# Kernel tuning notes

Hardware: AMD Instinct MI355X
Metric: run time of the kernel (lower is better)

The kernel has to match this reference:

```python
import jax, jax.numpy as jnp
import numpy as np
from jax.scipy.special import gammaln

NSTEP, NGRID, MU, LENF = 730, 1500, 16, 15
PRECS = 1e-5

# [low, high] physical ranges for the 12 HBV parameters (same order as torch code)
PARA_SCALE = np.array([[1, 6], [50, 1000], [0.05, 0.9], [0.01, 0.5], [0.001, 0.2],
                       [0.2, 1], [0, 10], [0, 100], [-2.5, 2.5], [0.5, 10],
                       [0, 0.1], [0, 0.2]], dtype=np.float32)
ROUT_SCALE = np.array([[0, 2.9], [0, 6.5]], dtype=np.float32)


def setup_inputs() -> dict:
    key = jax.random.key(0)
    kp, kt, ke, kpar, krt = jax.random.split(key, 5)
    P = jax.random.uniform(kp, (NSTEP, NGRID), jnp.float32) * 10.0   # precip mm/day
    T = jax.random.normal(kt, (NSTEP, NGRID), jnp.float32) * 8.0     # temp degC
    ETp = jax.random.uniform(ke, (NSTEP, NGRID), jnp.float32) * 5.0  # PET mm/day
    x = jnp.stack([P, T, ETp], axis=-1)                              # [Nstep, Ngrid, 3]
    parameters = jax.random.uniform(kpar, (NGRID, 12, MU), jnp.float32)
    rtwts = jax.random.uniform(krt, (NGRID, 2), jnp.float32)
    return {"x": x, "parameters": parameters, "rtwts": rtwts, "mu": MU}


def _hbv(x, parameters, rtwts, mu):
    Nstep, Ngrid = x.shape[0], x.shape[1]
    # scale raw [0,1] parameters into physical ranges; each is [Ngrid, mu]
    lo, hi = PARA_SCALE[:, 0], PARA_SCALE[:, 1]
    par = [lo[i] + parameters[:, i, :] * (hi[i] - lo[i]) for i in range(12)]
    (parBETA, parFC, parK0, parK1, parK2, parLP, parPERC, parUZL,
     parTT, parCFMAX, parCFR, parCWH) = par

    P, T, ETp = x[:, :, 0], x[:, :, 1], x[:, :, 2]  # each [Nstep, Ngrid]

    init = tuple(jnp.full((Ngrid, mu), 0.001, jnp.float32) for _ in range(5))

    def step(carry, inp):
        SNOWPACK, MELTWATER, SM, SUZ, SLZ = carry
        Pt, Tt, Et = inp
        Pm, Tm, ETpm = Pt[:, None], Tt[:, None], Et[:, None]  # [Ngrid, 1]
        is_rain = (Tm >= parTT).astype(jnp.float32)
        RAIN = Pm * is_rain
        SNOW = Pm * (1.0 - is_rain)
        SNOWPACK = SNOWPACK + SNOW
        melt = jnp.minimum(jnp.maximum(parCFMAX * (Tm - parTT), 0.0), SNOWPACK)
        MELTWATER = MELTWATER + melt
        SNOWPACK = SNOWPACK - melt
        refreezing = jnp.minimum(jnp.maximum(parCFR * parCFMAX * (parTT - Tm), 0.0), MELTWATER)
        SNOWPACK = SNOWPACK + refreezing
        MELTWATER = MELTWATER - refreezing
        tosoil = jnp.maximum(MELTWATER - parCWH * SNOWPACK, 0.0)
        MELTWATER = MELTWATER - tosoil
        soil_wetness = jnp.clip((SM / parFC) ** parBETA, 0.0, 1.0)
        recharge = (RAIN + tosoil) * soil_wetness
        SM = SM + RAIN + tosoil - recharge
        excess = jnp.maximum(SM - parFC, 0.0)
        SM = SM - excess
        evapfactor = jnp.clip(SM / (parLP * parFC), 0.0, 1.0)
        ETact = jnp.minimum(SM, ETpm * evapfactor)
        SM = jnp.maximum(SM - ETact, PRECS)
        SUZ = SUZ + recharge + excess
        PERC = jnp.minimum(SUZ, parPERC)
        SUZ = SUZ - PERC
        Q0 = parK0 * jnp.maximum(SUZ - parUZL, 0.0)
        SUZ = SUZ - Q0
        Q1 = parK1 * SUZ
        SUZ = SUZ - Q1
        SLZ = SLZ + PERC
        Q2 = parK2 * SLZ
        SLZ = SLZ - Q2
        return (SNOWPACK, MELTWATER, SM, SUZ, SLZ), (Q0 + Q1 + Q2, Q0, Q1, Q2, ETact)

    _, (Qsimmu, Q0s, Q1s, Q2s, ETmu) = jax.lax.scan(step, init, (P, T, ETp))

    Qsimave = Qsimmu.mean(-1)  # [Nstep, Ngrid]  (muwts is None)

    # gamma unit hydrograph routing (routOpt=True, comprout=False)
    tempa = ROUT_SCALE[0, 0] + rtwts[:, 0] * (ROUT_SCALE[0, 1] - ROUT_SCALE[0, 0])
    tempb = ROUT_SCALE[1, 0] + rtwts[:, 1] * (ROUT_SCALE[1, 1] - ROUT_SCALE[1, 0])
    aa = jnp.maximum(tempa, 0.0) + 0.1      # [Ngrid]
    theta = jnp.maximum(tempb, 0.0) + 0.5   # [Ngrid]
    t = jnp.arange(LENF, dtype=jnp.float32) + 0.5  # [lenF]
    # w[k, g] = t_k^(a-1) * exp(-t_k/theta) / (Gamma(a) * theta^a)
    w = (jnp.exp(-gammaln(aa))[None, :] * theta[None, :] ** (-aa[None, :])
         * t[:, None] ** (aa[None, :] - 1.0) * jnp.exp(-t[:, None] / theta[None, :]))
    w = w / w.sum(0)  # normalize over kernel axis -> [lenF, Ngrid]

    # causal depthwise conv over time: Qs[n,g] = sum_k w[k,g] * Qsimave[n-k,g]
    xpad = jnp.pad(Qsimave, ((LENF - 1, 0), (0, 0)))
    Qs = jnp.zeros_like(Qsimave)
    for k in range(LENF):
        Qs = Qs + w[k][None, :] * jax.lax.dynamic_slice_in_dim(xpad, LENF - 1 - k, Nstep, 0)
    Qs = Qs[..., None]  # [Nstep, Ngrid, 1]

    Qall = jnp.concatenate([Qs,
                            Q0s.mean(-1, keepdims=True),
                            Q1s.mean(-1, keepdims=True),
                            Q2s.mean(-1, keepdims=True),
                            ETmu.mean(-1, keepdims=True)], axis=-1)
    return Qall  # [Nstep, Ngrid, 5]


def reference(x, parameters, rtwts, mu):
    return _hbv(x, parameters, rtwts, mu)
```

## Files before the change

### kernel.cpp

```cpp
#include <hip/hip_runtime.h>
#include <math.h>

#define NSTEP  730
#define NGRID  1500
#define LENF   15
#define PRECS  1e-5f
#define CH     16
#define NCHUNK 46
#define NPHASE (NCHUNK+3)
#define QROW   260
#define OTW    21

static __device__ __forceinline__ float fast_pow01(float x, float y) {
    return __builtin_amdgcn_exp2f(y * __builtin_amdgcn_logf(x));
}

__global__ __launch_bounds__(256, 1)
void hbv_scan_kernel(const float* __restrict__ x,
                     const float* __restrict__ params,
                     const float* __restrict__ rtwts,
                     float* __restrict__ out)
{
    __shared__ float  xring[3*CH*16];
    __shared__ float  rtbuf[2*CH*64];
    __shared__ float2 soilbuf[2*CH*64];
    __shared__ float  qbuf[2*CH*QROW];
    __shared__ float  outtile[CH*OTW];
    __shared__ float  ring[4*64];

    const int tid  = threadIdx.x;
    const int wid  = tid >> 6;
    const int lane = tid & 63;
    const int gl = lane >> 4, m = lane & 15;
    const int b  = blockIdx.x;
    const int g  = b*4 + gl;
    const float inv16 = 1.f/16.f;

    if (wid == 3) {
        #pragma unroll
        for (int j = 0; j < 3; ++j) {
            const int idx = lane + 64*j;
            const int r = idx/12, rem = idx - 12*r;
            const int gi = rem/3, ch = rem - 3*gi;
            xring[r*16 + gi*4 + ch] = x[r*4500 + b*12 + gi*3 + ch];
        }
    }
    ring[tid & 255] = 0.f;
    __syncthreads();

    if (wid == 0) {
        const float pTT     = -2.5f + params[(g*12+8)*16+m]*5.f;
        const float pCFMAX  =  0.5f + params[(g*12+9)*16+m]*9.5f;
        const float pCFR    =          params[(g*12+10)*16+m]*0.1f;
        const float pCWH    =          params[(g*12+11)*16+m]*0.2f;
        const float refCoef = pCFR*pCFMAX;
        const float negCMTT = -pCFMAX*pTT;
        const float refCTT  = refCoef*pTT;
        float SP = 0.001f, MW = 0.001f;
        for (int p = 0; p < NPHASE; ++p) {
            if (p < NCHUNK) {
                const float* xb = &xring[(p%3)*CH*16 + gl*4];
                float* rb = &rtbuf[(p&1)*CH*64];
                #pragma unroll
                for (int s = 0; s < CH; ++s) {
                    const float2 PT = *(const float2*)(xb + s*16);
                    const float Pm = PT.x, Tm = PT.y;
                    const float RAIN    = (Tm >= pTT) ? Pm : 0.f;
                    const float SNOW    = Pm - RAIN;
                    const float meltcap = fmaxf(fmaf(pCFMAX, Tm, negCMTT), 0.f);
                    const float refcap  = fmaxf(fmaf(-refCoef, Tm, refCTT), 0.f);
                    const float SP1 = SP + SNOW;
                    const float melt = fminf(meltcap, SP1);
                    const float MW1 = MW + melt;
                    const float refreeze = fminf(refcap, MW1);
                    SP = SP1 - melt + refreeze;
                    const float MW2 = MW1 - refreeze;
                    const float tosoil = fmaxf(fmaf(-pCWH, SP, MW2), 0.f);
                    MW = MW2 - tosoil;
                    rb[s*64 + lane] = RAIN + tosoil;
                }
            }
            __syncthreads();
        }
    } else if (wid == 1) {
        const float pBETA = 1.f  + params[(g*12+0)*16+m]*5.f;
        const float pFC   = 50.f + params[(g*12+1)*16+m]*950.f;
        const float pLP   = 0.2f + params[(g*12+5)*16+m]*0.8f;
        const float invFC = 1.f/pFC, invLPFC = 1.f/(pLP*pFC);
        float SM = 0.001f;
        for (int p = 0; p < NPHASE; ++p) {
            if (p >= 1 && p-1 < NCHUNK) {
                const int c = p-1;
                const float* xe = &xring[(c%3)*CH*16 + gl*4 + 2];
                const float* rb = &rtbuf[(c&1)*CH*64];
                float2* sb = &soilbuf[(c&1)*CH*64];
                #pragma unroll
                for (int s = 0; s < CH; ++s) {
                    const float rt = rb[s*64 + lane];
                    const float Em = xe[s*16];
                    const float sw = fminf(fast_pow01(SM*invFC, pBETA), 1.f);
                    const float recharge = rt*sw;
                    const float SM1 = fmaf(rt, 1.f - sw, SM);
                    const float SM2 = fminf(SM1, pFC);
                    const float excess = SM1 - SM2;
                    const float evap = fminf(SM2*invLPFC, 1.f);
                    const float ETact = fminf(SM2, Em*evap);
                    SM = fmaxf(SM2 - ETact, PRECS);
                    sb[s*64 + lane] = make_float2(recharge + excess, ETact);
                }
            }
            __syncthreads();
        }
    } else if (wid == 2) {
        const float pK0   = 0.05f  + params[(g*12+2)*16+m]*0.85f;
        const float pK1   = 0.01f  + params[(g*12+3)*16+m]*0.49f;
        const float pK2   = 0.001f + params[(g*12+4)*16+m]*0.199f;
        const float pPERC =          params[(g*12+6)*16+m]*10.f;
        const float pUZL  =          params[(g*12+7)*16+m]*100.f;
        const float oneMinusK0 = 1.f - pK0, K0UZL = pK0*pUZL;
        float SUZ = 0.001f, SLZ = 0.001f;
        for (int p = 0; p < NPHASE; ++p) {
            if (p >= 2 && p-2 < NCHUNK) {
                const int c = p-2;
                const float2* sb = &soilbuf[(c&1)*CH*64];
                float* qb = &qbuf[(c&1)*CH*QROW];
                #pragma unroll
                for (int s = 0; s < CH; ++s) {
                    const float2 rE = sb[s*64 + lane];
                    const float SUZ1 = SUZ + rE.x;
                    const float SUZ2 = fmaxf(SUZ1 - pPERC, 0.f);
                    const float PERC = SUZ1 - SUZ2;
                    const float SUZ3 = fminf(SUZ2, fmaf(SUZ2, oneMinusK0, K0UZL));
                    const float Q0 = SUZ2 - SUZ3;
                    const float Q1 = pK1 * SUZ3;
                    SUZ = SUZ3 - Q1;
                    const float SLZ1 = SLZ + PERC;
                    const float Q2 = pK2 * SLZ1;
                    SLZ = SLZ1 - Q2;
                    *(float4*)&qb[s*QROW + lane*4] = make_float4(Q0, Q1, Q2, rE.y);
                }
            }
            __syncthreads();
        }
    } else {
        float wq[LENF];
        {
            const float ta  = rtwts[g*2+0] * 2.9f;
            const float tbv = rtwts[g*2+1] * 6.5f;
            const float aa = fmaxf(ta, 0.f) + 0.1f;
            const float th = fmaxf(tbv, 0.f) + 0.5f;
            const float c0v = expf(-lgammaf(aa)) * powf(th, -aa);
            float wsum = 0.f;
            #pragma unroll
            for (int k = 0; k < LENF; ++k) {
                const float tt = (float)k + 0.5f;
                wq[k] = c0v * powf(tt, aa-1.f) * expf(-tt/th);
                wsum += wq[k];
            }
            const float ws = inv16 / wsum;
            #pragma unroll
            for (int k = 0; k < LENF; ++k) wq[k] *= ws;
        }
        int rbase[3], bcol[3], lslot[3];
        #pragma unroll
        for (int j = 0; j < 3; ++j) {
            const int idx = lane + 64*j;
            const int r = idx/12, rem = idx - 12*r;
            const int gi = rem/3, ch = rem - 3*gi;
            rbase[j] = r;
            bcol[j]  = b*12 + gi*3 + ch;
            lslot[j] = r*16 + gi*4 + ch;
        }
        int st_o[5], st_g[5];
        #pragma unroll
        for (int j = 0; j < 5; ++j) {
            const int idx = lane + 64*j;
            const int tt = idx/20, cl = idx - 20*tt;
            st_o[j] = tt*OTW + cl;
            st_g[j] = tt*7500 + cl;
        }

        for (int p = 0; p < NPHASE; ++p) {
            const bool do_stage = (p+1 < NCHUNK);
            float stg0=0.f, stg1=0.f, stg2=0.f;
            if (do_stage) {
                int r0 = (p+1)*CH + rbase[0]; r0 = (r0 < NSTEP) ? r0 : (NSTEP-1);
                int r1 = (p+1)*CH + rbase[1]; r1 = (r1 < NSTEP) ? r1 : (NSTEP-1);
                int r2 = (p+1)*CH + rbase[2]; r2 = (r2 < NSTEP) ? r2 : (NSTEP-1);
                stg0 = x[r0*4500 + bcol[0]];
                stg1 = x[r1*4500 + bcol[1]];
                stg2 = x[r2*4500 + bcol[2]];
            }
            const int q = p - 3;
            if (q >= 0) {
                const int nstep = (q == NCHUNK-1) ? (NSTEP - (NCHUNK-1)*CH) : CH;
                const float* qb = &qbuf[(q&1)*CH*QROW];
                const int t = q*CH + m;
                float a0=0.f, a1=0.f, a2=0.f, a3=0.f;
                if (m < nstep) {
                    #pragma unroll
                    for (int i = 0; i < 16; ++i) {
                        const float4 v = *(const float4*)&qb[m*QROW + gl*64 + i*4];
                        a0 += v.x; a1 += v.y; a2 += v.z; a3 += v.w;
                    }
                    ring[gl*64 + (t & 63)] = a0 + a1 + a2;
                }
                asm volatile("s_waitcnt lgkmcnt(0)" ::: "memory");
                if (m < nstep) {
                    float acc = 0.f;
                    #pragma unroll
                    for (int k = 0; k < LENF; ++k)
                        acc += wq[k] * ring[gl*64 + ((t - k) & 63)];
                    float* ot = &outtile[m*OTW + gl*5];
                    ot[0] = acc;
                    ot[1] = a0*inv16; ot[2] = a1*inv16;
                    ot[3] = a2*inv16; ot[4] = a3*inv16;
                }
                asm volatile("s_waitcnt lgkmcnt(0)" ::: "memory");
                const int ndw = nstep*20;
                float* ob = out + q*CH*7500 + b*20;
                #pragma unroll
                for (int j = 0; j < 5; ++j) {
                    const int idx = lane + 64*j;
                    if (idx < ndw) ob[st_g[j]] = outtile[st_o[j]];
                }
            }
            if (do_stage) {
                float* xd = &xring[((p+1)%3)*CH*16];
                xd[lslot[0]] = stg0; xd[lslot[1]] = stg1; xd[lslot[2]] = stg2;
            }
            __syncthreads();
        }
    }
}

extern "C" void kernel_launch(void* const* d_in, const int* in_sizes, int n_in,
                              void* d_out, int out_size, void* d_ws, size_t ws_size,
                              hipStream_t stream)
{
    const float* x      = (const float*)d_in[0];
    const float* params = (const float*)d_in[1];
    const float* rt     = (const float*)d_in[2];
    float* out = (float*)d_out;

    dim3 grid(NGRID / 4), block(256);
    hipLaunchKernelGGL(hbv_scan_kernel, grid, block, 0, stream, x, params, rt, out);
}
```

Measured before the change: 61.08 us.

## Replace block barriers with LDS flag-based producer/consumer sync between warp stages

```diff
diff --git a/kernel.cpp b/kernel.cpp
--- a/kernel.cpp
+++ b/kernel.cpp
@@ -7,12 +7,30 @@
 #define PRECS  1e-5f
 #define CH     16
 #define NCHUNK 46
-#define NPHASE (NCHUNK+3)
 #define QROW   260
 #define OTW    21
 
+#define F_XPROD 0
+#define F_XCA   1
+#define F_XCB   2
+#define F_RTP   3
+#define F_RTC   4
+#define F_SP    5
+#define F_SC    6
+#define F_QP    7
+#define F_QC    8
+
 static __device__ __forceinline__ float fast_pow01(float x, float y) {
     return __builtin_amdgcn_exp2f(y * __builtin_amdgcn_logf(x));
+}
+static __device__ __forceinline__ void wait_ge(volatile int* f, int v) {
+    if (v <= 0) return;
+    while (*f < v) __builtin_amdgcn_s_sleep(1);
+    asm volatile("" ::: "memory");
+}
+static __device__ __forceinline__ void publish(volatile int* f, int v, bool leader) {
+    asm volatile("s_waitcnt lgkmcnt(0)" ::: "memory");
+    if (leader) *f = v;
 }
 
 __global__ __launch_bounds__(256, 1)
@@ -27,6 +45,7 @@
     __shared__ float  qbuf[2*CH*QROW];
     __shared__ float  outtile[CH*OTW];
     __shared__ float  ring[4*64];
+    __shared__ int    flags[16];
 
     const int tid  = threadIdx.x;
     const int wid  = tid >> 6;
@@ -34,18 +53,12 @@
     const int gl = lane >> 4, m = lane & 15;
     const int b  = blockIdx.x;
     const int g  = b*4 + gl;
+    const bool leader = (lane == 0);
     const float inv16 = 1.f/16.f;
-
-    if (wid == 3) {
-        #pragma unroll
-        for (int j = 0; j < 3; ++j) {
-            const int idx = lane + 64*j;
-            const int r = idx/12, rem = idx - 12*r;
-            const int gi = rem/3, ch = rem - 3*gi;
-            xring[r*16 + gi*4 + ch] = x[r*4500 + b*12 + gi*3 + ch];
-        }
-    }
-    ring[tid & 255] = 0.f;
+    volatile int* fl = flags;
+
+    if (tid < 16) flags[tid] = 0;
+    ring[tid] = 0.f;
     __syncthreads();
 
     if (wid == 0) {
@@ -57,30 +70,31 @@
         const float negCMTT = -pCFMAX*pTT;
         const float refCTT  = refCoef*pTT;
         float SP = 0.001f, MW = 0.001f;
-        for (int p = 0; p < NPHASE; ++p) {
-            if (p < NCHUNK) {
-                const float* xb = &xring[(p%3)*CH*16 + gl*4];
-                float* rb = &rtbuf[(p&1)*CH*64];
-                #pragma unroll
-                for (int s = 0; s < CH; ++s) {
-                    const float2 PT = *(const float2*)(xb + s*16);
-                    const float Pm = PT.x, Tm = PT.y;
-                    const float RAIN    = (Tm >= pTT) ? Pm : 0.f;
-                    const float SNOW    = Pm - RAIN;
-                    const float meltcap = fmaxf(fmaf(pCFMAX, Tm, negCMTT), 0.f);
-                    const float refcap  = fmaxf(fmaf(-refCoef, Tm, refCTT), 0.f);
-                    const float SP1 = SP + SNOW;
-                    const float melt = fminf(meltcap, SP1);
-                    const float MW1 = MW + melt;
-                    const float refreeze = fminf(refcap, MW1);
-                    SP = SP1 - melt + refreeze;
-                    const float MW2 = MW1 - refreeze;
-                    const float tosoil = fmaxf(fmaf(-pCWH, SP, MW2), 0.f);
-                    MW = MW2 - tosoil;
-                    rb[s*64 + lane] = RAIN + tosoil;
-                }
-            }
-            __syncthreads();
+        for (int c = 0; c < NCHUNK; ++c) {
+            wait_ge(&fl[F_XPROD], c+1);
+            wait_ge(&fl[F_RTC],   c-1);
+            const float* xb = &xring[(c%3)*CH*16 + gl*4];
+            float* rb = &rtbuf[(c&1)*CH*64 + lane];
+            #pragma unroll
+            for (int s = 0; s < CH; ++s) {
+                const float2 PT = *(const float2*)(xb + s*16);
+                const float Pm = PT.x, Tm = PT.y;
+                const float RAIN    = (Tm >= pTT) ? Pm : 0.f;
+                const float SNOW    = Pm - RAIN;
+                const float meltcap = fmaxf(fmaf(pCFMAX, Tm, negCMTT), 0.f);
+                const float refcap  = fmaxf(fmaf(-refCoef, Tm, refCTT), 0.f);
+                const float SP1 = SP + SNOW;
+                const float melt = fminf(meltcap, SP1);
+                const float MW1 = MW + melt;
+                const float refreeze = fminf(refcap, MW1);
+                SP = SP1 - melt + refreeze;
+                const float MW2 = MW1 - refreeze;
+                const float tosoil = fmaxf(fmaf(-pCWH, SP, MW2), 0.f);
+                MW = MW2 - tosoil;
+                rb[s*64] = RAIN + tosoil;
+            }
+            publish(&fl[F_RTP], c+1, leader);
+            publish(&fl[F_XCA], c+1, leader);
         }
     } else if (wid == 1) {
         const float pBETA = 1.f  + params[(g*12+0)*16+m]*5.f;
@@ -88,28 +102,29 @@
         const float pLP   = 0.2f + params[(g*12+5)*16+m]*0.8f;
         const float invFC = 1.f/pFC, invLPFC = 1.f/(pLP*pFC);
         float SM = 0.001f;
-        for (int p = 0; p < NPHASE; ++p) {
-            if (p >= 1 && p-1 < NCHUNK) {
-                const int c = p-1;
-                const float* xe = &xring[(c%3)*CH*16 + gl*4 + 2];
-                const float* rb = &rtbuf[(c&1)*CH*64];
-                float2* sb = &soilbuf[(c&1)*CH*64];
-                #pragma unroll
-                for (int s = 0; s < CH; ++s) {
-                    const float rt = rb[s*64 + lane];
-                    const float Em = xe[s*16];
-                    const float sw = fminf(fast_pow01(SM*invFC, pBETA), 1.f);
-                    const float recharge = rt*sw;
-                    const float SM1 = fmaf(rt, 1.f - sw, SM);
-                    const float SM2 = fminf(SM1, pFC);
-                    const float excess = SM1 - SM2;
-                    const float evap = fminf(SM2*invLPFC, 1.f);
-                    const float ETact = fminf(SM2, Em*evap);
-                    SM = fmaxf(SM2 - ETact, PRECS);
-                    sb[s*64 + lane] = make_float2(recharge + excess, ETact);
-                }
-            }
-            __syncthreads();
+        for (int c = 0; c < NCHUNK; ++c) {
+            wait_ge(&fl[F_RTP], c+1);
+            wait_ge(&fl[F_SC],  c-1);
+            const float* xe = &xring[(c%3)*CH*16 + gl*4 + 2];
+            const float* rb = &rtbuf[(c&1)*CH*64 + lane];
+            float2* sb = &soilbuf[(c&1)*CH*64 + lane];
+            #pragma unroll
+            for (int s = 0; s < CH; ++s) {
+                const float rt = rb[s*64];
+                const float Em = xe[s*16];
+                const float cE = Em * invLPFC;
+                const float SMprt = SM + rt;
+                const float sw = fast_pow01(SM*invFC, pBETA);
+                const float SM1 = fmaf(-rt, sw, SMprt);
+                const float SM2 = fminf(SM1, pFC);
+                const float ETact = fminf(fminf(SM2*cE, SM2), Em);
+                const float re = fmaf(rt, sw, SM1 - SM2);
+                SM = fmaxf(SM2 - ETact, PRECS);
+                sb[s*64] = make_float2(re, ETact);
+            }
+            publish(&fl[F_SP],  c+1, leader);
+            publish(&fl[F_XCB], c+1, leader);
+            publish(&fl[F_RTC], c+1, leader);
         }
     } else if (wid == 2) {
         const float pK0   = 0.05f  + params[(g*12+2)*16+m]*0.85f;
@@ -119,28 +134,28 @@
         const float pUZL  =          params[(g*12+7)*16+m]*100.f;
         const float oneMinusK0 = 1.f - pK0, K0UZL = pK0*pUZL;
         float SUZ = 0.001f, SLZ = 0.001f;
-        for (int p = 0; p < NPHASE; ++p) {
-            if (p >= 2 && p-2 < NCHUNK) {
-                const int c = p-2;
-                const float2* sb = &soilbuf[(c&1)*CH*64];
-                float* qb = &qbuf[(c&1)*CH*QROW];
-                #pragma unroll
-                for (int s = 0; s < CH; ++s) {
-                    const float2 rE = sb[s*64 + lane];
-                    const float SUZ1 = SUZ + rE.x;
-                    const float SUZ2 = fmaxf(SUZ1 - pPERC, 0.f);
-                    const float PERC = SUZ1 - SUZ2;
-                    const float SUZ3 = fminf(SUZ2, fmaf(SUZ2, oneMinusK0, K0UZL));
-                    const float Q0 = SUZ2 - SUZ3;
-                    const float Q1 = pK1 * SUZ3;
-                    SUZ = SUZ3 - Q1;
-                    const float SLZ1 = SLZ + PERC;
-                    const float Q2 = pK2 * SLZ1;
-                    SLZ = SLZ1 - Q2;
-                    *(float4*)&qb[s*QROW + lane*4] = make_float4(Q0, Q1, Q2, rE.y);
-                }
-            }
-            __syncthreads();
+        for (int c = 0; c < NCHUNK; ++c) {
+            wait_ge(&fl[F_SP], c+1);
+            wait_ge(&fl[F_QC], c-1);
+            const float2* sb = &soilbuf[(c&1)*CH*64 + lane];
+            float* qb = &qbuf[(c&1)*CH*QROW + lane*4];
+            #pragma unroll
+            for (int s = 0; s < CH; ++s) {
+                const float2 rE = sb[s*64];
+                const float SUZ1 = SUZ + rE.x;
+                const float SUZ2 = fmaxf(SUZ1 - pPERC, 0.f);
+                const float PERC = SUZ1 - SUZ2;
+                const float SUZ3 = fminf(SUZ2, fmaf(SUZ2, oneMinusK0, K0UZL));
+                const float Q0 = SUZ2 - SUZ3;
+                const float Q1 = pK1 * SUZ3;
+                SUZ = SUZ3 - Q1;
+                const float SLZ1 = SLZ + PERC;
+                const float Q2 = pK2 * SLZ1;
+                SLZ = SLZ1 - Q2;
+                *(float4*)(qb + s*QROW) = make_float4(Q0, Q1, Q2, rE.y);
+            }
+            publish(&fl[F_QP], c+1, leader);
+            publish(&fl[F_SC], c+1, leader);
         }
     } else {
         float wq[LENF];
@@ -180,19 +195,40 @@
             st_g[j] = tt*7500 + cl;
         }
 
-        for (int p = 0; p < NPHASE; ++p) {
-            const bool do_stage = (p+1 < NCHUNK);
-            float stg0=0.f, stg1=0.f, stg2=0.f;
-            if (do_stage) {
-                int r0 = (p+1)*CH + rbase[0]; r0 = (r0 < NSTEP) ? r0 : (NSTEP-1);
-                int r1 = (p+1)*CH + rbase[1]; r1 = (r1 < NSTEP) ? r1 : (NSTEP-1);
-                int r2 = (p+1)*CH + rbase[2]; r2 = (r2 < NSTEP) ? r2 : (NSTEP-1);
-                stg0 = x[r0*4500 + bcol[0]];
-                stg1 = x[r1*4500 + bcol[1]];
-                stg2 = x[r2*4500 + bcol[2]];
-            }
-            const int q = p - 3;
-            if (q >= 0) {
+        float stg[3];
+        #pragma unroll
+        for (int j = 0; j < 3; ++j) stg[j] = x[rbase[j]*4500 + bcol[j]];
+        asm volatile("s_waitcnt vmcnt(0)" ::: "memory");
+        {
+            float* xd = &xring[0];
+            xd[lslot[0]] = stg[0]; xd[lslot[1]] = stg[1]; xd[lslot[2]] = stg[2];
+        }
+        publish(&fl[F_XPROD], 1, leader);
+        #pragma unroll
+        for (int j = 0; j < 3; ++j) {
+            int rr = CH + rbase[j]; rr = (rr < NSTEP) ? rr : (NSTEP-1);
+            stg[j] = x[rr*4500 + bcol[j]];
+        }
+
+        for (int q = 0; q < NCHUNK; ++q) {
+            if (q+1 < NCHUNK) {
+                asm volatile("s_waitcnt vmcnt(0)" ::: "memory");
+                float* xd = &xring[((q+1)%3)*CH*16];
+                xd[lslot[0]] = stg[0]; xd[lslot[1]] = stg[1]; xd[lslot[2]] = stg[2];
+                publish(&fl[F_XPROD], q+2, leader);
+            }
+            if (q+2 < NCHUNK) {
+                wait_ge(&fl[F_XCA], q);
+                wait_ge(&fl[F_XCB], q);
+                #pragma unroll
+                for (int j = 0; j < 3; ++j) {
+                    int rr = (q+2)*CH + rbase[j];
+                    rr = (rr < NSTEP) ? rr : (NSTEP-1);
+                    stg[j] = x[rr*4500 + bcol[j]];
+                }
+            }
+            wait_ge(&fl[F_QP], q+1);
+            {
                 const int nstep = (q == NCHUNK-1) ? (NSTEP - (NCHUNK-1)*CH) : CH;
                 const float* qb = &qbuf[(q&1)*CH*QROW];
                 const int t = q*CH + m;
@@ -225,11 +261,7 @@
                     if (idx < ndw) ob[st_g[j]] = outtile[st_o[j]];
                 }
             }
-            if (do_stage) {
-                float* xd = &xring[((p+1)%3)*CH*16];
-                xd[lslot[0]] = stg0; xd[lslot[1]] = stg1; xd[lslot[2]] = stg2;
-            }
-            __syncthreads();
+            publish(&fl[F_QC], q+1, leader);
         }
     }
 }
```

Result: slower. 102.4 us (+67.7%).
